# Kernel tuning notes

Hardware: AMD Instinct MI355X
Metric: run time of the kernel (lower is better)

Reference implementation:

```python
import jax, jax.numpy as jnp
import numpy as np

PREVIOUS_VISIT = 64


def setup_inputs() -> dict:
    key = jax.random.key(0)
    k1, k2, k3, k4 = jax.random.split(key, 4)
    B, T, D, H = 1024, 64, 512, 512
    scale = 1.0 / np.sqrt(D)
    return {
        "input_context": jax.random.normal(k1, (B, T, D), dtype=jnp.float32),
        "kernel": jax.random.normal(k2, (D, 4 * H), dtype=jnp.float32) * scale,
        "recurrent_kernel": jax.random.normal(k3, (H, 4 * H), dtype=jnp.float32) * scale,
        "bias": jax.random.normal(k4, (4 * H,), dtype=jnp.float32) * 0.01,
    }


def reference(input_context, kernel, recurrent_kernel, bias):
    # Keras LSTMCell unrolled over PREVIOUS_VISIT steps; gate order i, f, c, o.
    B = input_context.shape[0]
    H = recurrent_kernel.shape[0]
    xs = jnp.transpose(input_context[:, :PREVIOUS_VISIT, :], (1, 0, 2))  # [T, B, D]

    def step(carry, xt):
        h, c = carry
        z = xt @ kernel + h @ recurrent_kernel + bias  # [B, 4H]
        i, f, g, o = jnp.split(z, 4, axis=-1)
        i = jax.nn.sigmoid(i)
        f = jax.nn.sigmoid(f)
        g = jnp.tanh(g)
        o = jax.nn.sigmoid(o)
        c_new = f * c + i * g
        h_new = o * jnp.tanh(c_new)
        return (h_new, c_new), h_new

    init = (jnp.zeros((B, H), dtype=input_context.dtype),
            jnp.zeros((B, H), dtype=input_context.dtype))
    _, hs = jax.lax.scan(step, init, xs)  # hs: [T, B, H]
    return jnp.transpose(hs, (1, 0, 2))  # [B, T, H]
```

## Files before the change

kernel.cpp:

```cpp
#include <hip/hip_runtime.h>
#include <hip/hip_bf16.h>
#include <hip/hip_fp16.h>


typedef __attribute__((ext_vector_type(8))) short bfrag8;
typedef __attribute__((ext_vector_type(4))) float facc4;
typedef __attribute__((ext_vector_type(4))) unsigned int u32x4;

#define MFMA_B16(a, b, c) __builtin_amdgcn_mfma_f32_16x16x32_bf16(a, b, c, 0, 0, 0)

__device__ __forceinline__ unsigned short f2bf(float f) {
  unsigned int u = __float_as_uint(f);
  u += 0x7FFFu + ((u >> 16) & 1u);
  return (unsigned short)(u >> 16);
}
__device__ __forceinline__ float sigm(float x)  { return 1.0f / (1.0f + __expf(-x)); }
__device__ __forceinline__ float tanh_(float x) { return 1.0f - 2.0f / (__expf(2.0f * x) + 1.0f); }

__device__ __forceinline__ void gl2lds16(const void* g, void* l) {
  __builtin_amdgcn_global_load_lds(
      (const __attribute__((address_space(1))) unsigned int*)g,
      (__attribute__((address_space(3))) unsigned int*)l, 16, 0, 0);
}

__device__ __forceinline__ u32x4 ld128_coh(const void* p) {
  u32x4 r;
  asm volatile("global_load_dwordx4 %0, %1, off sc0 sc1" : "=v"(r) : "v"(p));
  return r;
}
__device__ __forceinline__ void st128_coh(void* p, u32x4 v) {
  asm volatile("global_store_dwordx4 %0, %1, off sc0 sc1" :: "v"(p), "v"(v) : "memory");
}

__device__ __forceinline__ int foff(int row, int seg) {
  return (row << 7) + ((((seg & 8) | ((seg ^ row) & 7))) << 3);
}


__global__ void prep_w(const float* __restrict__ Wk, const float* __restrict__ Wr,
                       const float* __restrict__ bias,
                       unsigned short* __restrict__ Wx, unsigned short* __restrict__ Wh,
                       float* __restrict__ biasr, unsigned int* __restrict__ cnt)
{
  int gid = (blockIdx.x << 8) + threadIdx.x;
  int k   = gid >> 11;
  int col = gid & 2047;
  float v = (k < 512) ? Wk[((size_t)k << 11) + col]
                      : Wr[((size_t)(k - 512) << 11) + col];
  int n = ((col & 511) << 2) | (col >> 9);
  if (k < 512) Wx[((size_t)n << 9) + k]         = f2bf(v);
  else         Wh[((size_t)n << 9) + (k - 512)] = f2bf(v);
  if (gid < 2048) biasr[((gid & 511) << 2) | (gid >> 9)] = bias[gid];
  if (gid < 4096) cnt[gid] = 0u;
}

__global__ void prep_x(const float* __restrict__ x, unsigned short* __restrict__ Xbf)
{
  int flat = (blockIdx.x << 8) + threadIdx.x;
  int d8 = flat & 63;
  int b  = (flat >> 6) & 1023;
  int t  = flat >> 16;
  const float* src = x + ((((size_t)b << 6) + t) << 9) + (d8 << 3);
  float4 v0 = *(const float4*)src;
  float4 v1 = *(const float4*)(src + 4);
  uint4 u;
  u.x = f2bf(v0.x) | ((unsigned)f2bf(v0.y) << 16);
  u.y = f2bf(v0.z) | ((unsigned)f2bf(v0.w) << 16);
  u.z = f2bf(v1.x) | ((unsigned)f2bf(v1.y) << 16);
  u.w = f2bf(v1.z) | ((unsigned)f2bf(v1.w) << 16);
  *(uint4*)&Xbf[((((size_t)t << 10) + b) << 9) + (d8 << 3)] = u;
}

__global__ __launch_bounds__(256, 3)
void zx_gemm(const unsigned short* __restrict__ Xbf, const unsigned short* __restrict__ Wx,
             unsigned short* __restrict__ zx)
{
  __shared__ __align__(16) unsigned short As[8192];
  __shared__ __align__(16) unsigned short Bs[8192];
  __shared__ float Zs[64][68];

  const int tid  = threadIdx.x;
  const int lane = tid & 63;
  const int w    = tid >> 6;
  const int llo  = lane & 15;
  const int lhi  = lane >> 4;
  const int wm   = (w >> 1) & 1;
  const int wn   = w & 1;

  const int n0 = blockIdx.x << 6;
  const int by = blockIdx.y;
  const int t  = by >> 4;
  const int b0 = (by & 15) << 6;

  facc4 acc00 = {0.f,0.f,0.f,0.f};
  facc4 acc01 = acc00, acc10 = acc00, acc11 = acc00;

  const int am0 = (wm << 5) + llo;
  const int bn0 = (wn << 5) + llo;

  for (int ci = 0; ci < 4; ++ci) {
    const int kb = ci << 7;
#pragma unroll
    for (int j = 0; j < 4; ++j) {
      int p = (j << 8) + tid;
      int r = p >> 4, ps = p & 15;
      int s = (ps & 8) | ((ps ^ r) & 7);
      gl2lds16(Xbf + ((((size_t)t << 10) + (b0 + r)) << 9) + kb + (s << 3), &As[p << 3]);
      gl2lds16(Wx  + (((size_t)(n0 + r)) << 9) + kb + (s << 3),             &Bs[p << 3]);
    }
    __syncthreads();
#pragma unroll
    for (int kk = 0; kk < 4; ++kk) {
      const int s0 = (kk << 2) + lhi;
      bfrag8 a0 = *(const bfrag8*)&As[foff(am0,      s0)];
      bfrag8 a1 = *(const bfrag8*)&As[foff(am0 + 16, s0)];
      bfrag8 b0 = *(const bfrag8*)&Bs[foff(bn0,      s0)];
      bfrag8 b1 = *(const bfrag8*)&Bs[foff(bn0 + 16, s0)];
      acc00 = MFMA_B16(a0, b0, acc00);
      acc01 = MFMA_B16(a0, b1, acc01);
      acc10 = MFMA_B16(a1, b0, acc10);
      acc11 = MFMA_B16(a1, b1, acc11);
    }
    __syncthreads();
  }

#pragma unroll
  for (int rr = 0; rr < 4; ++rr) {
    int rbase = (wm << 5) + (lhi << 2) + rr;
    int cbase = (wn << 5) + llo;
    Zs[rbase][cbase]           = acc00[rr];
    Zs[rbase][cbase + 16]      = acc01[rr];
    Zs[rbase + 16][cbase]      = acc10[rr];
    Zs[rbase + 16][cbase + 16] = acc11[rr];
  }
  __syncthreads();

  const int hs = tid & 15;
  const int rw = tid >> 4;
#pragma unroll
  for (int it = 0; it < 4; ++it) {
    int row = rw + (it << 4);
    float4 z = *(const float4*)&Zs[row][hs << 2];
    ushort4 o;
    o.x = __half_as_ushort(__float2half(z.x));
    o.y = __half_as_ushort(__float2half(z.y));
    o.z = __half_as_ushort(__float2half(z.z));
    o.w = __half_as_ushort(__float2half(z.w));
    *(ushort4*)&zx[((((size_t)t << 10) + (b0 + row)) << 11) + n0 + (hs << 2)] = o;
  }
}

__global__ __launch_bounds__(256, 1)
void lstm_persist(unsigned short* __restrict__ Hbuf,
                  const unsigned short* __restrict__ Wh,
                  const unsigned short* __restrict__ zx,
                  const float* __restrict__ biasr,
                  float* __restrict__ out,
                  unsigned int* __restrict__ cnt)
{
  extern __shared__ __align__(16) char smem_raw[];
  unsigned short* Bs = (unsigned short*)smem_raw;
  unsigned short* As = (unsigned short*)(smem_raw + 131072);
  unsigned short* Sc = (unsigned short*)(smem_raw + 147456);

  const int tid  = threadIdx.x;
  const int lane = tid & 63;
  const int w    = tid >> 6;
  const int llo  = lane & 15;
  const int lhi  = lane >> 4;

  const int bx  = blockIdx.x;
  const int nbI = bx & 15;
  const int mg  = bx >> 4;
  const int m0  = mg << 6;
  const int n0  = nbI << 7;
  const int hb  = nbI << 5;

  for (int i = 0; i < 32; ++i) {
    int p  = (i << 8) + tid;
    int ci = p >> 11;
    int q  = p & 2047;
    int r  = q >> 4, ps = q & 15;
    int s  = (ps & 8) | ((ps ^ r) & 7);
    gl2lds16(Wh + (((size_t)(n0 + r)) << 9) + (ci << 7) + (s << 3), Bs + ((size_t)p << 3));
  }

  const int nw0 = w << 5;
  float4 bb[2];
  bb[0] = *(const float4*)&biasr[(size_t)(hb + (w << 3) + 0 + lhi) << 2];
  bb[1] = *(const float4*)&biasr[(size_t)(hb + (w << 3) + 4 + lhi) << 2];

  float c[2][4] = {{0.f,0.f,0.f,0.f},{0.f,0.f,0.f,0.f}};

  asm volatile("s_waitcnt vmcnt(0)" ::: "memory");
  __syncthreads();

  const size_t HSTG = (size_t)16 * 1024 * 32;

  for (int t = 0; t < 64; ++t) {
    const unsigned short* zxt = zx + ((size_t)t << 21);

    ushort4 zp[2][4];
#pragma unroll
    for (int nt = 0; nt < 2; ++nt)
#pragma unroll
      for (int bt = 0; bt < 4; ++bt) {
        int b = m0 + (bt << 4) + llo;
        int h = hb + (w << 3) + (nt << 2) + lhi;
        zp[nt][bt] = *(const ushort4*)&zxt[((size_t)b << 11) + (h << 2)];
      }

    facc4 acc[2][4];
#pragma unroll
    for (int nt = 0; nt < 2; ++nt)
#pragma unroll
      for (int bt = 0; bt < 4; ++bt)
        acc[nt][bt] = (facc4){0.f, 0.f, 0.f, 0.f};

    if (t) {
      if (tid < 4) {
        const unsigned int* cp = cnt + (t << 6) + (mg << 2) + tid;
        while (__hip_atomic_load(cp, __ATOMIC_RELAXED, __HIP_MEMORY_SCOPE_AGENT) < 4u)
          __builtin_amdgcn_s_sleep(1);
      }
      __syncthreads();

      const unsigned short* Hs = Hbuf + (size_t)(t & 3) * HSTG;
      u32x4 av[16];
#pragma unroll
      for (int ci = 0; ci < 4; ++ci)
#pragma unroll
        for (int j = 0; j < 4; ++j) {
          int p = (j << 8) + tid;
          int r = p >> 4, ps = p & 15;
          int s = (ps & 8) | ((ps ^ r) & 7);
          int nbp = (ci << 2) + (s >> 2);
          av[(ci << 2) + j] =
              ld128_coh(Hs + ((size_t)nbp << 15) + ((size_t)(m0 + r) << 5) + ((s & 3) << 3));
        }
#pragma unroll
      for (int ci = 0; ci < 4; ++ci) {
        if      (ci == 0) asm volatile("s_waitcnt vmcnt(12)" ::: "memory");
        else if (ci == 1) asm volatile("s_waitcnt vmcnt(8)"  ::: "memory");
        else if (ci == 2) asm volatile("s_waitcnt vmcnt(4)"  ::: "memory");
        else              asm volatile("s_waitcnt vmcnt(0)"  ::: "memory");
        __builtin_amdgcn_sched_barrier(0);
#pragma unroll
        for (int j = 0; j < 4; ++j) {
          int p = (j << 8) + tid;
          *(u32x4*)&As[(size_t)p << 3] = av[(ci << 2) + j];
        }
        __syncthreads();
#pragma unroll
        for (int kk = 0; kk < 4; ++kk) {
          const int s0 = (kk << 2) + lhi;
          bfrag8 wh0 = *(const bfrag8*)&Bs[(ci << 14) + foff(nw0 + llo,      s0)];
          bfrag8 wh1 = *(const bfrag8*)&Bs[(ci << 14) + foff(nw0 + 16 + llo, s0)];
#pragma unroll
          for (int bt = 0; bt < 4; ++bt) {
            bfrag8 hf = *(const bfrag8*)&As[foff((bt << 4) + llo, s0)];
            acc[0][bt] = MFMA_B16(wh0, hf, acc[0][bt]);
            acc[1][bt] = MFMA_B16(wh1, hf, acc[1][bt]);
          }
        }
        __syncthreads();
      }
    }

    float hn_s[2][4];
#pragma unroll
    for (int nt = 0; nt < 2; ++nt)
#pragma unroll
      for (int bt = 0; bt < 4; ++bt) {
        float zi = acc[nt][bt][0] + __half2float(__ushort_as_half(zp[nt][bt].x)) + bb[nt].x;
        float zf = acc[nt][bt][1] + __half2float(__ushort_as_half(zp[nt][bt].y)) + bb[nt].y;
        float zg = acc[nt][bt][2] + __half2float(__ushort_as_half(zp[nt][bt].z)) + bb[nt].z;
        float zo = acc[nt][bt][3] + __half2float(__ushort_as_half(zp[nt][bt].w)) + bb[nt].w;
        float ig = sigm(zi);
        float fg = sigm(zf);
        float gg = tanh_(zg);
        float og = sigm(zo);
        float cn = fg * c[nt][bt] + ig * gg;
        c[nt][bt] = cn;
        float hn = og * tanh_(cn);
        hn_s[nt][bt] = hn;
        Sc[(w << 9) + (((bt << 4) + llo) << 3) + (nt << 2) + lhi] = f2bf(hn);
      }
    __syncthreads();

    if (t < 63) {
      u32x4 hv = *(const u32x4*)&Sc[((tid & 3) << 9) + ((tid >> 2) << 3)];
      unsigned short* Hn = Hbuf + (size_t)((t + 1) & 3) * HSTG;
      st128_coh(Hn + ((size_t)nbI << 15) + ((size_t)(m0 + (tid >> 2)) << 5) + ((tid & 3) << 3), hv);
    }
#pragma unroll
    for (int nt = 0; nt < 2; ++nt)
#pragma unroll
      for (int bt = 0; bt < 4; ++bt) {
        int b = m0 + (bt << 4) + llo;
        int h = hb + (w << 3) + (nt << 2) + lhi;
        out[((size_t)b << 15) + ((size_t)t << 9) + h] = hn_s[nt][bt];
      }
    if (t < 63) {
      if (t == 0) asm volatile("s_waitcnt vmcnt(0)" ::: "memory");
      else        asm volatile("s_waitcnt vmcnt(8)" ::: "memory");
      __syncthreads();
      if (tid == 0)
        __hip_atomic_fetch_add(&cnt[((t + 1) << 6) + (mg << 2) + (nbI >> 2)], 1u,
                               __ATOMIC_RELAXED, __HIP_MEMORY_SCOPE_AGENT);
    }
  }
}

extern "C" void kernel_launch(void* const* d_in, const int* in_sizes, int n_in,
                              void* d_out, int out_size, void* d_ws, size_t ws_size,
                              hipStream_t stream) {
  const float* x    = (const float*)d_in[0];
  const float* Wk   = (const float*)d_in[1];
  const float* Wr   = (const float*)d_in[2];
  const float* bias = (const float*)d_in[3];
  float* out = (float*)d_out;

  char* ws = (char*)d_ws;
  unsigned short* Wx    = (unsigned short*)(ws);
  unsigned short* Wh    = (unsigned short*)(ws + (2u << 20));
  float*          biasr = (float*)(ws + (4u << 20));
  unsigned int*   cnt   = (unsigned int*)(ws + (4u << 20) + 8192);
  unsigned short* Hbuf  = (unsigned short*)(ws + (5u << 20));
  unsigned short* Xbf   = (unsigned short*)(ws + (9u << 20));
  unsigned short* zx    = (unsigned short*)(ws + (73u << 20));

  (void)hipFuncSetAttribute((const void*)lstm_persist,
                            hipFuncAttributeMaxDynamicSharedMemorySize, 151552);

  prep_w<<<dim3(8192), dim3(256), 0, stream>>>(Wk, Wr, bias, Wx, Wh, biasr, cnt);
  prep_x<<<dim3(16384), dim3(256), 0, stream>>>(x, Xbf);
  zx_gemm<<<dim3(32, 1024), dim3(256), 0, stream>>>(Xbf, Wx, zx);
  lstm_persist<<<dim3(256), dim3(256), 151552, stream>>>(Hbuf, Wh, zx, biasr, out, cnt);
}
```

Measured before the change: 1.164 ms.

## Load h fragments directly into MFMA registers, removing the LDS staging of H

Reorganizes the persistent LSTM kernel so each wave owns 16 batch rows across all 128 gate columns instead of a 2x4 tile. The global H buffer layout changes to a fragment-ready order, so loaded 128-bit vectors are used directly as MFMA B operands. This drops the As shared-memory staging and the two __syncthreads per k-chunk. Bias moves to LDS. Each wave now reads 8 W fragments per k-step instead of 2, which raises LDS read traffic for the weights.

```diff
diff --git a/kernel.cpp b/kernel.cpp
--- a/kernel.cpp
+++ b/kernel.cpp
@@ -159,9 +159,9 @@
                   unsigned int* __restrict__ cnt)
 {
   extern __shared__ __align__(16) char smem_raw[];
-  unsigned short* Bs = (unsigned short*)smem_raw;
-  unsigned short* As = (unsigned short*)(smem_raw + 131072);
-  unsigned short* Sc = (unsigned short*)(smem_raw + 147456);
+  unsigned short* Bs   = (unsigned short*)smem_raw;
+  unsigned short* Sc   = (unsigned short*)(smem_raw + 131072);
+  float*          Bias = (float*)(smem_raw + 135168);
 
   const int tid  = threadIdx.x;
   const int lane = tid & 63;
@@ -184,38 +184,30 @@
     int s  = (ps & 8) | ((ps ^ r) & 7);
     gl2lds16(Wh + (((size_t)(n0 + r)) << 9) + (ci << 7) + (s << 3), Bs + ((size_t)p << 3));
   }
-
-  const int nw0 = w << 5;
-  float4 bb[2];
-  bb[0] = *(const float4*)&biasr[(size_t)(hb + (w << 3) + 0 + lhi) << 2];
-  bb[1] = *(const float4*)&biasr[(size_t)(hb + (w << 3) + 4 + lhi) << 2];
-
-  float c[2][4] = {{0.f,0.f,0.f,0.f},{0.f,0.f,0.f,0.f}};
+  if (tid < 128) Bias[tid] = biasr[((size_t)hb << 2) + tid];
+
+  float c[8];
+#pragma unroll
+  for (int i = 0; i < 8; ++i) c[i] = 0.f;
+
+  const int bmine = m0 + (w << 4) + llo;
 
   asm volatile("s_waitcnt vmcnt(0)" ::: "memory");
   __syncthreads();
 
-  const size_t HSTG = (size_t)16 * 1024 * 32;
+  const size_t HSTG = (size_t)16 * 64 * 64 * 8;
 
   for (int t = 0; t < 64; ++t) {
     const unsigned short* zxt = zx + ((size_t)t << 21);
 
-    ushort4 zp[2][4];
-#pragma unroll
-    for (int nt = 0; nt < 2; ++nt)
-#pragma unroll
-      for (int bt = 0; bt < 4; ++bt) {
-        int b = m0 + (bt << 4) + llo;
-        int h = hb + (w << 3) + (nt << 2) + lhi;
-        zp[nt][bt] = *(const ushort4*)&zxt[((size_t)b << 11) + (h << 2)];
-      }
-
-    facc4 acc[2][4];
-#pragma unroll
-    for (int nt = 0; nt < 2; ++nt)
-#pragma unroll
-      for (int bt = 0; bt < 4; ++bt)
-        acc[nt][bt] = (facc4){0.f, 0.f, 0.f, 0.f};
+    ushort4 zp[8];
+#pragma unroll
+    for (int nt = 0; nt < 8; ++nt)
+      zp[nt] = *(const ushort4*)&zxt[((size_t)bmine << 11) + ((hb + (nt << 2) + lhi) << 2)];
+
+    facc4 acc[8];
+#pragma unroll
+    for (int nt = 0; nt < 8; ++nt) acc[nt] = (facc4){0.f, 0.f, 0.f, 0.f};
 
     if (t) {
       if (tid < 4) {
@@ -225,18 +217,15 @@
       }
       __syncthreads();
 
-      const unsigned short* Hs = Hbuf + (size_t)(t & 3) * HSTG;
+      const unsigned short* Hs = Hbuf + (size_t)(t & 3) * HSTG + ((size_t)mg << 15);
+
       u32x4 av[16];
 #pragma unroll
       for (int ci = 0; ci < 4; ++ci)
 #pragma unroll
         for (int j = 0; j < 4; ++j) {
-          int p = (j << 8) + tid;
-          int r = p >> 4, ps = p & 15;
-          int s = (ps & 8) | ((ps ^ r) & 7);
-          int nbp = (ci << 2) + (s >> 2);
-          av[(ci << 2) + j] =
-              ld128_coh(Hs + ((size_t)nbp << 15) + ((size_t)(m0 + r) << 5) + ((s & 3) << 3));
+          int kseg = (ci << 4) + (j << 2) + lhi;
+          av[(ci << 2) + j] = ld128_coh(Hs + (((kseg << 6) + (w << 4) + llo) << 3));
         }
 #pragma unroll
       for (int ci = 0; ci < 4; ++ci) {
@@ -246,61 +235,46 @@
         else              asm volatile("s_waitcnt vmcnt(0)"  ::: "memory");
         __builtin_amdgcn_sched_barrier(0);
 #pragma unroll
-        for (int j = 0; j < 4; ++j) {
-          int p = (j << 8) + tid;
-          *(u32x4*)&As[(size_t)p << 3] = av[(ci << 2) + j];
-        }
-        __syncthreads();
-#pragma unroll
         for (int kk = 0; kk < 4; ++kk) {
+          bfrag8 hf = __builtin_bit_cast(bfrag8, av[(ci << 2) + kk]);
           const int s0 = (kk << 2) + lhi;
-          bfrag8 wh0 = *(const bfrag8*)&Bs[(ci << 14) + foff(nw0 + llo,      s0)];
-          bfrag8 wh1 = *(const bfrag8*)&Bs[(ci << 14) + foff(nw0 + 16 + llo, s0)];
-#pragma unroll
-          for (int bt = 0; bt < 4; ++bt) {
-            bfrag8 hf = *(const bfrag8*)&As[foff((bt << 4) + llo, s0)];
-            acc[0][bt] = MFMA_B16(wh0, hf, acc[0][bt]);
-            acc[1][bt] = MFMA_B16(wh1, hf, acc[1][bt]);
+#pragma unroll
+          for (int nt = 0; nt < 8; ++nt) {
+            bfrag8 wh = *(const bfrag8*)&Bs[(ci << 14) + foff((nt << 4) + llo, s0)];
+            acc[nt] = MFMA_B16(wh, hf, acc[nt]);
           }
         }
-        __syncthreads();
       }
     }
 
-    float hn_s[2][4];
-#pragma unroll
-    for (int nt = 0; nt < 2; ++nt)
-#pragma unroll
-      for (int bt = 0; bt < 4; ++bt) {
-        float zi = acc[nt][bt][0] + __half2float(__ushort_as_half(zp[nt][bt].x)) + bb[nt].x;
-        float zf = acc[nt][bt][1] + __half2float(__ushort_as_half(zp[nt][bt].y)) + bb[nt].y;
-        float zg = acc[nt][bt][2] + __half2float(__ushort_as_half(zp[nt][bt].z)) + bb[nt].z;
-        float zo = acc[nt][bt][3] + __half2float(__ushort_as_half(zp[nt][bt].w)) + bb[nt].w;
-        float ig = sigm(zi);
-        float fg = sigm(zf);
-        float gg = tanh_(zg);
-        float og = sigm(zo);
-        float cn = fg * c[nt][bt] + ig * gg;
-        c[nt][bt] = cn;
-        float hn = og * tanh_(cn);
-        hn_s[nt][bt] = hn;
-        Sc[(w << 9) + (((bt << 4) + llo) << 3) + (nt << 2) + lhi] = f2bf(hn);
-      }
+    float hn_s[8];
+#pragma unroll
+    for (int nt = 0; nt < 8; ++nt) {
+      float4 bbv = *(const float4*)&Bias[((nt << 2) + lhi) << 2];
+      float zi = acc[nt][0] + __half2float(__ushort_as_half(zp[nt].x)) + bbv.x;
+      float zf = acc[nt][1] + __half2float(__ushort_as_half(zp[nt].y)) + bbv.y;
+      float zg = acc[nt][2] + __half2float(__ushort_as_half(zp[nt].z)) + bbv.z;
+      float zo = acc[nt][3] + __half2float(__ushort_as_half(zp[nt].w)) + bbv.w;
+      float ig = sigm(zi);
+      float fg = sigm(zf);
+      float gg = tanh_(zg);
+      float og = sigm(zo);
+      float cn = fg * c[nt] + ig * gg;
+      c[nt] = cn;
+      float hn = og * tanh_(cn);
+      hn_s[nt] = hn;
+      Sc[((nt >> 1) << 9) + (((w << 4) + llo) << 3) + ((nt & 1) << 2) + lhi] = f2bf(hn);
+    }
     __syncthreads();
 
     if (t < 63) {
-      u32x4 hv = *(const u32x4*)&Sc[((tid & 3) << 9) + ((tid >> 2) << 3)];
-      unsigned short* Hn = Hbuf + (size_t)((t + 1) & 3) * HSTG;
-      st128_coh(Hn + ((size_t)nbI << 15) + ((size_t)(m0 + (tid >> 2)) << 5) + ((tid & 3) << 3), hv);
-    }
-#pragma unroll
-    for (int nt = 0; nt < 2; ++nt)
-#pragma unroll
-      for (int bt = 0; bt < 4; ++bt) {
-        int b = m0 + (bt << 4) + llo;
-        int h = hb + (w << 3) + (nt << 2) + lhi;
-        out[((size_t)b << 15) + ((size_t)t << 9) + h] = hn_s[nt][bt];
-      }
+      u32x4 hv = *(const u32x4*)&Sc[((tid >> 6) << 9) + ((tid & 63) << 3)];
+      unsigned short* Hn = Hbuf + (size_t)((t + 1) & 3) * HSTG + ((size_t)mg << 15);
+      st128_coh(Hn + (((((nbI << 2) + (tid >> 6)) << 6) + (tid & 63)) << 3), hv);
+    }
+#pragma unroll
+    for (int nt = 0; nt < 8; ++nt)
+      out[((size_t)bmine << 15) + ((size_t)t << 9) + hb + (nt << 2) + lhi] = hn_s[nt];
     if (t < 63) {
       if (t == 0) asm volatile("s_waitcnt vmcnt(0)" ::: "memory");
       else        asm volatile("s_waitcnt vmcnt(8)" ::: "memory");
@@ -331,10 +305,10 @@
   unsigned short* zx    = (unsigned short*)(ws + (73u << 20));
 
   (void)hipFuncSetAttribute((const void*)lstm_persist,
-                            hipFuncAttributeMaxDynamicSharedMemorySize, 151552);
+                            hipFuncAttributeMaxDynamicSharedMemorySize, 135680);
 
   prep_w<<<dim3(8192), dim3(256), 0, stream>>>(Wk, Wr, bias, Wx, Wh, biasr, cnt);
   prep_x<<<dim3(16384), dim3(256), 0, stream>>>(x, Xbf);
   zx_gemm<<<dim3(32, 1024), dim3(256), 0, stream>>>(Xbf, Wx, zx);
-  lstm_persist<<<dim3(256), dim3(256), 151552, stream>>>(Hbuf, Wh, zx, biasr, out, cnt);
-}
+  lstm_persist<<<dim3(256), dim3(256), 135680, stream>>>(Hbuf, Wh, zx, biasr, out, cnt);
+}
```

Result: no change. 1.147 ms (-1.4%).
